# Optimization experiments

Measured on AMD Instinct MI355X. Metric: run time of the kernel, lower is better.

Reference implementation:

```python
import jax, jax.numpy as jnp
import numpy as np

D_K = 64  # hardcoded in the original module
NEG_INF = -1.0e9


def setup_inputs() -> dict:
    key = jax.random.key(0)
    kq, kk, kv = jax.random.split(key, 3)
    B, H, S, D = 2, 16, 2048, D_K
    Q = jax.random.normal(kq, (B, H, S, D), dtype=jnp.float32)
    K = jax.random.normal(kk, (B, H, S, D), dtype=jnp.float32)
    V = jax.random.normal(kv, (B, H, S, D), dtype=jnp.float32)
    # causal mask: True means masked out (matches masked_fill_ semantics)
    causal = jnp.triu(jnp.ones((S, S), dtype=jnp.bool_), k=1)
    attn_mask = jnp.broadcast_to(causal, (B, H, S, S))
    return {"Q": Q, "K": K, "V": V, "attn_mask": attn_mask}


def reference(Q, K, V, attn_mask):
    # scores = Q @ (K^T / sqrt(d_k))
    scale = 1.0 / np.sqrt(D_K).astype(np.float32)
    scores = jnp.einsum("bhqd,bhkd->bhqk", Q, K * scale)  # [B,H,S,S]
    scores = jnp.where(attn_mask, NEG_INF, scores)
    attn_scores = jax.nn.softmax(scores, axis=-1)
    context = jnp.einsum("bhqk,bhkd->bhqd", attn_scores, V)
    return (context, attn_scores)
```

## Files before the change

kernel.cpp:

```cpp
#include <hip/hip_runtime.h>
#include <stdint.h>

typedef float  f32x4  __attribute__((ext_vector_type(4)));
typedef short  s16x4  __attribute__((ext_vector_type(4)));
typedef short  s16x8  __attribute__((ext_vector_type(8)));

#define S_LEN 2048
#define D_K   64
#define NBH   32
#define VT_STRIDE (S_LEN + 32)
#define MFMA  __builtin_amdgcn_mfma_f32_16x16x32_bf16

__device__ __forceinline__ short f2bf(float f) {
    uint32_t u = __builtin_bit_cast(uint32_t, f);
    u += 0x7fffu + ((u >> 16) & 1u);
    return (short)(u >> 16);
}
__device__ __forceinline__ float bf2f(short s) {
    uint32_t u = ((uint32_t)(uint16_t)s) << 16;
    return __builtin_bit_cast(float, u);
}
__device__ __forceinline__ s16x4 cvt4(float4 f) {
    s16x4 r; r[0] = f2bf(f.x); r[1] = f2bf(f.y); r[2] = f2bf(f.z); r[3] = f2bf(f.w);
    return r;
}
__device__ __forceinline__ s16x8 cat(s16x4 a, s16x4 b) {
    return __builtin_shufflevector(a, b, 0, 1, 2, 3, 4, 5, 6, 7);
}
__device__ __forceinline__ void nt_store4(float* p, f32x4 v) {
    __builtin_nontemporal_store(v, (f32x4*)p);
}

__global__ __launch_bounds__(256) void preconv(
    const float* __restrict__ K, const float* __restrict__ V,
    short* __restrict__ Kb, short* __restrict__ VT)
{
    const int bh  = blockIdx.x >> 6;
    const int seg = blockIdx.x & 63;
    const int tid = threadIdx.x;
    const float* Ks = K + ((size_t)bh * S_LEN + seg * 32) * D_K;
    const float* Vs = V + ((size_t)bh * S_LEN + seg * 32) * D_K;
    short* Kd  = Kb + ((size_t)bh * S_LEN + seg * 32) * D_K;
    short* VTd = VT + (size_t)bh * D_K * VT_STRIDE + seg * 32;

    for (int i = tid; i < 512; i += 256) {
        const int r = i >> 4, ci = i & 15;
        float4 f = *(const float4*)(Ks + r * D_K + (ci << 2));
        const int jj = ((ci & 3) << 1) + ((ci >> 2) & 1) + ((ci >> 3) << 3);
        *(s16x4*)(Kd + r * D_K + (jj << 2)) = cvt4(f);
    }
    for (int i = tid; i < 512; i += 256) {
        const int r = i & 31, c = (i >> 5) << 2;
        float4 f = *(const float4*)(Vs + r * D_K + c);
        const int rp = (((r & 15) >> 2) << 3) + (((r >> 4) & 1) << 2) + (r & 3);
        VTd[(size_t)(c + 0) * VT_STRIDE + rp] = f2bf(f.x);
        VTd[(size_t)(c + 1) * VT_STRIDE + rp] = f2bf(f.y);
        VTd[(size_t)(c + 2) * VT_STRIDE + rp] = f2bf(f.z);
        VTd[(size_t)(c + 3) * VT_STRIDE + rp] = f2bf(f.w);
    }
}

#define SSTR 2056
__global__ __launch_bounds__(256) void attn_sp(
    const float* __restrict__ Q, const short* __restrict__ Kb,
    const short* __restrict__ VT, float* __restrict__ outC,
    float* __restrict__ outS)
{
    __shared__ __align__(16) char smem[32 * SSTR * 2];
    __shared__ float lbuf[4][32];

    const int tid = threadIdx.x, lane = tid & 63, wv = tid >> 6;
    const int xcd = blockIdx.x & 7;
    const int idx = blockIdx.x >> 3;
    const int bh  = (xcd << 2) + (idx >> 6);
    const int j   = 63 - (idx & 63);
    const int q0  = j << 5;
    const int l15 = lane & 15;
    const int g   = lane >> 4;
    const int d0  = g << 2;
    const int qa  = q0 + l15;

    const short* Kbh = Kb + (size_t)bh * S_LEN * D_K;
    const short* VTh = VT + (size_t)bh * D_K * VT_STRIDE;
    float* outSb = outS + (size_t)bh * S_LEN * S_LEN;
    float* outCb = outC + (size_t)bh * S_LEN * D_K;
    short* sstash = (short*)smem;

    s16x8 qf0a, qf1a, qf0b, qf1b;
    {
        const float4* qp = (const float4*)(Q + ((size_t)bh * S_LEN + qa) * D_K);
        qf0a = cat(cvt4(qp[g]),     cvt4(qp[g + 4]));
        qf1a = cat(cvt4(qp[g + 8]), cvt4(qp[g + 12]));
        const float4* qp2 = (const float4*)(Q + ((size_t)bh * S_LEN + qa + 16) * D_K);
        qf0b = cat(cvt4(qp2[g]),     cvt4(qp2[g + 4]));
        qf1b = cat(cvt4(qp2[g + 8]), cvt4(qp2[g + 12]));
    }

    const int ntiles = j + 1;
    const float scale = 0.125f;

    float la = 0.f, lb = 0.f;
    f32x4 z4 = {0.f,0.f,0.f,0.f};
    f32x4 cxa0 = z4, cxa1 = z4, cxa2 = z4, cxa3 = z4;
    f32x4 cxb0 = z4, cxb1 = z4, cxb2 = z4, cxb3 = z4;
    {
        s16x8 k0[4], v0[4], k1[4], v1[4];

        auto LDK = [&](s16x8* kk, s16x8* vv, int t) {
            const short* kp = Kbh + (((size_t)t << 5) + l15) * D_K + (g << 3);
            kk[0] = *(const s16x8*)(kp);
            kk[1] = *(const s16x8*)(kp + 32);
            kk[2] = *(const s16x8*)(kp + 16 * D_K);
            kk[3] = *(const s16x8*)(kp + 16 * D_K + 32);
            const short* vp = VTh + (size_t)l15 * VT_STRIDE + (t << 5) + (g << 3);
            vv[0] = *(const s16x8*)(vp);
            vv[1] = *(const s16x8*)(vp + 16 * VT_STRIDE);
            vv[2] = *(const s16x8*)(vp + 32 * VT_STRIDE);
            vv[3] = *(const s16x8*)(vp + 48 * VT_STRIDE);
        };
        auto CMPS = [&](const s16x8* kk, const s16x8* vv, int T) {
            f32x4 sa0 = z4, sa1 = z4, sb0 = z4, sb1 = z4;
            sa0 = MFMA(kk[0], qf0a, sa0, 0,0,0);
            sa0 = MFMA(kk[1], qf1a, sa0, 0,0,0);
            sa1 = MFMA(kk[2], qf0a, sa1, 0,0,0);
            sa1 = MFMA(kk[3], qf1a, sa1, 0,0,0);
            sb0 = MFMA(kk[0], qf0b, sb0, 0,0,0);
            sb0 = MFMA(kk[1], qf1b, sb0, 0,0,0);
            sb1 = MFMA(kk[2], qf0b, sb1, 0,0,0);
            sb1 = MFMA(kk[3], qf1b, sb1, 0,0,0);
            s16x8 pfa, pfb;
            if (T < j) {
                #pragma unroll
                for (int r = 0; r < 4; ++r) {
                    float e;
                    e = __expf(sa0[r] * scale); la += e; pfa[r]   = f2bf(e);
                    e = __expf(sa1[r] * scale); la += e; pfa[4+r] = f2bf(e);
                    e = __expf(sb0[r] * scale); lb += e; pfb[r]   = f2bf(e);
                    e = __expf(sb1[r] * scale); lb += e; pfb[4+r] = f2bf(e);
                }
            } else {
                #pragma unroll
                for (int r = 0; r < 4; ++r) {
                    const bool c = (d0 + r) <= l15;
                    float e;
                    e = c ? __expf(sa0[r] * scale) : 0.f; la += e; pfa[r] = f2bf(e);
                    pfa[4+r] = 0;
                    e = __expf(sb0[r] * scale);           lb += e; pfb[r] = f2bf(e);
                    e = c ? __expf(sb1[r] * scale) : 0.f; lb += e; pfb[4+r] = f2bf(e);
                }
            }
            const int cbase = (T << 5) + d0;
            short* sA = &sstash[l15 * SSTR + cbase];
            *(s16x4*)(sA)      = __builtin_shufflevector(pfa, pfa, 0, 1, 2, 3);
            *(s16x4*)(sA + 16) = __builtin_shufflevector(pfa, pfa, 4, 5, 6, 7);
            short* sB = &sstash[(16 + l15) * SSTR + cbase];
            *(s16x4*)(sB)      = __builtin_shufflevector(pfb, pfb, 0, 1, 2, 3);
            *(s16x4*)(sB + 16) = __builtin_shufflevector(pfb, pfb, 4, 5, 6, 7);
            cxa0 = MFMA(pfa, vv[0], cxa0, 0,0,0);
            cxa1 = MFMA(pfa, vv[1], cxa1, 0,0,0);
            cxa2 = MFMA(pfa, vv[2], cxa2, 0,0,0);
            cxa3 = MFMA(pfa, vv[3], cxa3, 0,0,0);
            cxb0 = MFMA(pfb, vv[0], cxb0, 0,0,0);
            cxb1 = MFMA(pfb, vv[1], cxb1, 0,0,0);
            cxb2 = MFMA(pfb, vv[2], cxb2, 0,0,0);
            cxb3 = MFMA(pfb, vv[3], cxb3, 0,0,0);
        };

        int t = wv;
        if (t < ntiles) {
            LDK(k0, v0, t);
            while (t + 4 < ntiles) {
                LDK(k1, v1, t + 4);
                CMPS(k0, v0, t);
                t += 4;
                if (t + 4 < ntiles) {
                    LDK(k0, v0, t + 4);
                    CMPS(k1, v1, t);
                    t += 4;
                } else {
                    CMPS(k1, v1, t);
                    t += 4;
                    break;
                }
            }
            if (t < ntiles) CMPS(k0, v0, t);
        }
    }
    la += __shfl_xor(la, 16); la += __shfl_xor(la, 32);
    lb += __shfl_xor(lb, 16); lb += __shfl_xor(lb, 32);
    if (lane < 16) { lbuf[wv][l15] = la; lbuf[wv][16 + l15] = lb; }
    __syncthreads();
    #pragma unroll
    for (int r = 0; r < 4; ++r) {
        const float ra = 1.f / (lbuf[0][d0 + r] + lbuf[1][d0 + r]
                              + lbuf[2][d0 + r] + lbuf[3][d0 + r]);
        const float rb = 1.f / (lbuf[0][16 + d0 + r] + lbuf[1][16 + d0 + r]
                              + lbuf[2][16 + d0 + r] + lbuf[3][16 + d0 + r]);
        cxa0[r] *= ra; cxa1[r] *= ra; cxa2[r] *= ra; cxa3[r] *= ra;
        cxb0[r] *= rb; cxb1[r] *= rb; cxb2[r] *= rb; cxb3[r] *= rb;
    }

    const int kz = ntiles << 5;
    {
        #pragma unroll
        for (int rr8 = 0; rr8 < 8; ++rr8) {
            const int row = (wv << 3) + rr8;
            const float rinv_r = 1.f /
                (lbuf[0][row] + lbuf[1][row] + lbuf[2][row] + lbuf[3][row]);
            float* rowp = outSb + (size_t)(q0 + row) * S_LEN;
            const short* srow = &sstash[row * SSTR];
            for (int c = lane << 2; c < S_LEN; c += 256) {
                f32x4 v;
                if (c < kz) {
                    s16x4 sv = *(const s16x4*)(srow + c);
                    v[0] = bf2f(sv[0]) * rinv_r;
                    v[1] = bf2f(sv[1]) * rinv_r;
                    v[2] = bf2f(sv[2]) * rinv_r;
                    v[3] = bf2f(sv[3]) * rinv_r;
                } else {
                    v[0] = 0.f; v[1] = 0.f; v[2] = 0.f; v[3] = 0.f;
                }
                nt_store4(rowp + c, v);
            }
        }
    }

    __syncthreads();
    {
        float* cb2 = (float*)smem;
        const int base = wv * 2080;
        #pragma unroll
        for (int r = 0; r < 4; ++r) {
            cb2[base + (d0 + r) * 65 +  0 + l15] = cxa0[r];
            cb2[base + (d0 + r) * 65 + 16 + l15] = cxa1[r];
            cb2[base + (d0 + r) * 65 + 32 + l15] = cxa2[r];
            cb2[base + (d0 + r) * 65 + 48 + l15] = cxa3[r];
            cb2[base + (16 + d0 + r) * 65 +  0 + l15] = cxb0[r];
            cb2[base + (16 + d0 + r) * 65 + 16 + l15] = cxb1[r];
            cb2[base + (16 + d0 + r) * 65 + 32 + l15] = cxb2[r];
            cb2[base + (16 + d0 + r) * 65 + 48 + l15] = cxb3[r];
        }
        __syncthreads();
        const int dbase = (tid & 15) << 2;
        for (int rr = tid >> 4; rr < 32; rr += 16) {
            f32x4 acc = *(const f32x4*)&cb2[0 * 2080 + rr * 65 + dbase];
            #pragma unroll
            for (int w = 1; w < 4; ++w) {
                f32x4 p = *(const f32x4*)&cb2[w * 2080 + rr * 65 + dbase];
                acc[0] += p[0]; acc[1] += p[1]; acc[2] += p[2]; acc[3] += p[3];
            }
            *(f32x4*)(outCb + (size_t)(q0 + rr) * D_K + dbase) = acc;
        }
    }
}

#define KSTRIDE 68
#define VSTRIDE 36
__global__ __launch_bounds__(256) void attn_causal_fb(
    const float* __restrict__ Q, const float* __restrict__ K,
    const float* __restrict__ V, float* __restrict__ outC,
    float* __restrict__ outS)
{
    __shared__ short Klds[32 * KSTRIDE];
    __shared__ short Vlds[64 * VSTRIDE];
    const int bh = blockIdx.x >> 5, q0 = (blockIdx.x & 31) << 6;
    const int tid = threadIdx.x, lane = tid & 63, wv = tid >> 6;
    const int q0w = q0 + (wv << 4), l15 = lane & 15, d0 = (lane >> 4) << 2;
    const int qg = q0w + l15, qhi = q0w + 15;
    const float* Kb = K + (size_t)bh * S_LEN * D_K;
    const float* Vb = V + (size_t)bh * S_LEN * D_K;
    float* outSb = outS + (size_t)bh * S_LEN * S_LEN;
    float* outCb = outC + (size_t)bh * S_LEN * D_K;
    s16x8 qf0, qf1;
    {
        const float4* qp = (const float4*)(Q + ((size_t)bh * S_LEN + qg) * D_K);
        qf0 = cat(cvt4(qp[d0 >> 2]), cvt4(qp[(d0 + 16) >> 2]));
        qf1 = cat(cvt4(qp[(d0 + 32) >> 2]), cvt4(qp[(d0 + 48) >> 2]));
    }
    const int npairs = (q0 >> 5) + 2;
    const float scale = 0.125f;
    float lsum = 0.f;
    for (int p = 0; p < npairs; ++p) {
        const int k0 = p << 5;
        for (int i = tid; i < 512; i += 256) {
            const int r = i >> 4, c = (i & 15) << 2;
            float4 f = *(const float4*)(Kb + (size_t)(k0 + r) * D_K + c);
            *(s16x4*)&Klds[r * KSTRIDE + c] = cvt4(f);
        }
        __syncthreads();
        if (k0 <= qhi) {
            #pragma unroll
            for (int s = 0; s < 2; ++s) {
                const short* kp = &Klds[(16 * s + l15) * KSTRIDE + d0];
                s16x8 a0 = cat(*(const s16x4*)kp, *(const s16x4*)(kp + 16));
                s16x8 a1 = cat(*(const s16x4*)(kp + 32), *(const s16x4*)(kp + 48));
                f32x4 c1 = {0.f,0.f,0.f,0.f};
                c1 = MFMA(a0, qf0, c1, 0,0,0);
                c1 = MFMA(a1, qf1, c1, 0,0,0);
                const int kbase = k0 + 16 * s + d0;
                #pragma unroll
                for (int r = 0; r < 4; ++r)
                    if (kbase + r <= qg) lsum += __expf(c1[r] * scale);
            }
        }
        __syncthreads();
    }
    lsum += __shfl_xor(lsum, 16);
    lsum += __shfl_xor(lsum, 32);
    const float rinv = 1.f / lsum;
    f32x4 ctx[4] = {{0,0,0,0},{0,0,0,0},{0,0,0,0},{0,0,0,0}};
    for (int p = 0; p < npairs; ++p) {
        const int k0 = p << 5;
        for (int i = tid; i < 512; i += 256) {
            const int r = i >> 4, c = (i & 15) << 2;
            float4 f = *(const float4*)(Kb + (size_t)(k0 + r) * D_K + c);
            *(s16x4*)&Klds[r * KSTRIDE + c] = cvt4(f);
            float4 gg = *(const float4*)(Vb + (size_t)(k0 + r) * D_K + c);
            Vlds[(c + 0) * VSTRIDE + r] = f2bf(gg.x);
            Vlds[(c + 1) * VSTRIDE + r] = f2bf(gg.y);
            Vlds[(c + 2) * VSTRIDE + r] = f2bf(gg.z);
            Vlds[(c + 3) * VSTRIDE + r] = f2bf(gg.w);
        }
        __syncthreads();
        if (k0 <= qhi) {
            s16x8 pf;
            #pragma unroll
            for (int s = 0; s < 2; ++s) {
                const short* kp = &Klds[(16 * s + l15) * KSTRIDE + d0];
                s16x8 a0 = cat(*(const s16x4*)kp, *(const s16x4*)(kp + 16));
                s16x8 a1 = cat(*(const s16x4*)(kp + 32), *(const s16x4*)(kp + 48));
                f32x4 c1 = {0.f,0.f,0.f,0.f};
                c1 = MFMA(a0, qf0, c1, 0,0,0);
                c1 = MFMA(a1, qf1, c1, 0,0,0);
                const int kbase = k0 + 16 * s + d0;
                f32x4 pw;
                #pragma unroll
                for (int r = 0; r < 4; ++r) {
                    float pe = (kbase + r <= qg) ? __expf(c1[r] * scale) * rinv : 0.f;
                    pw[r] = pe;
                    pf[4 * s + r] = f2bf(pe);
                }
                *(f32x4*)(outSb + (size_t)qg * S_LEN + kbase) = pw;
            }
            #pragma unroll
            for (int db = 0; db < 4; ++db) {
                const short* vp = &Vlds[(db * 16 + l15) * VSTRIDE + d0];
                s16x8 b = cat(*(const s16x4*)vp, *(const s16x4*)(vp + 16));
                ctx[db] = MFMA(pf, b, ctx[db], 0,0,0);
            }
        }
        __syncthreads();
    }
    #pragma unroll
    for (int db = 0; db < 4; ++db)
        #pragma unroll
        for (int r = 0; r < 4; ++r)
            outCb[(size_t)(q0w + d0 + r) * D_K + db * 16 + l15] = ctx[db][r];
    const int kz = ((qhi >> 5) + 1) << 5;
    const f32x4 z = {0.f,0.f,0.f,0.f};
    for (int r = 0; r < 16; ++r) {
        float* rowp = outSb + (size_t)(q0w + r) * S_LEN;
        for (int k = kz + (lane << 2); k < S_LEN; k += 256)
            *(f32x4*)(rowp + k) = z;
    }
}

extern "C" void kernel_launch(void* const* d_in, const int* in_sizes, int n_in,
                              void* d_out, int out_size, void* d_ws, size_t ws_size,
                              hipStream_t stream) {
    const float* Q = (const float*)d_in[0];
    const float* K = (const float*)d_in[1];
    const float* V = (const float*)d_in[2];
    float* outC = (float*)d_out;
    float* outS = (float*)d_out + (size_t)NBH * S_LEN * D_K;

    const size_t kb_elems = (size_t)NBH * S_LEN * D_K;
    const size_t vt_elems = (size_t)NBH * D_K * VT_STRIDE;
    const size_t need = (kb_elems + vt_elems) * sizeof(short);

    if (ws_size >= need) {
        short* Kb = (short*)d_ws;
        short* VT = Kb + kb_elems;
        preconv<<<dim3(NBH * 64), dim3(256), 0, stream>>>(K, V, Kb, VT);
        attn_sp<<<dim3(2048), dim3(256), 0, stream>>>(Q, Kb, VT, outC, outS);
    } else {
        attn_causal_fb<<<dim3(1024), dim3(256), 0, stream>>>(Q, K, V, outC, outS);
    }
}
```

Measured before the change: 147.1 us.

## Use eight waves per block to split key tiles in attention kernel

Doubles the attention block from 4 to 8 wavefronts, so each block of 32 query rows splits the key tiles across 8 waves instead of 4. The row-sum reduction, score write-out (4 rows per wave), and context reduction are rewritten for 8 partial accumulators. The context reduction runs in two phases through the shared buffer. The aim is more latency hiding and more parallelism per block on the causal workload. The cost is extra reduction and sync overhead, and possibly lower occupancy given the large shared-memory stash.

Measured after the change: 148.1 us. No clear change (+0.7%).

```diff
diff --git a/kernel.cpp b/kernel.cpp
--- a/kernel.cpp
+++ b/kernel.cpp
@@ -61,13 +61,13 @@
 }
 
 #define SSTR 2056
-__global__ __launch_bounds__(256) void attn_sp(
+__global__ __launch_bounds__(512) void attn_sp8(
     const float* __restrict__ Q, const short* __restrict__ Kb,
     const short* __restrict__ VT, float* __restrict__ outC,
     float* __restrict__ outS)
 {
     __shared__ __align__(16) char smem[32 * SSTR * 2];
-    __shared__ float lbuf[4][32];
+    __shared__ float lbuf[8][32];
 
     const int tid = threadIdx.x, lane = tid & 63, wv = tid >> 6;
     const int xcd = blockIdx.x & 7;
@@ -169,17 +169,17 @@
         int t = wv;
         if (t < ntiles) {
             LDK(k0, v0, t);
-            while (t + 4 < ntiles) {
-                LDK(k1, v1, t + 4);
+            while (t + 8 < ntiles) {
+                LDK(k1, v1, t + 8);
                 CMPS(k0, v0, t);
-                t += 4;
-                if (t + 4 < ntiles) {
-                    LDK(k0, v0, t + 4);
+                t += 8;
+                if (t + 8 < ntiles) {
+                    LDK(k0, v0, t + 8);
                     CMPS(k1, v1, t);
-                    t += 4;
+                    t += 8;
                 } else {
                     CMPS(k1, v1, t);
-                    t += 4;
+                    t += 8;
                     break;
                 }
             }
@@ -192,10 +192,13 @@
     __syncthreads();
     #pragma unroll
     for (int r = 0; r < 4; ++r) {
-        const float ra = 1.f / (lbuf[0][d0 + r] + lbuf[1][d0 + r]
-                              + lbuf[2][d0 + r] + lbuf[3][d0 + r]);
-        const float rb = 1.f / (lbuf[0][16 + d0 + r] + lbuf[1][16 + d0 + r]
-                              + lbuf[2][16 + d0 + r] + lbuf[3][16 + d0 + r]);
+        float sa = 0.f, sb = 0.f;
+        #pragma unroll
+        for (int w = 0; w < 8; ++w) {
+            sa += lbuf[w][d0 + r];
+            sb += lbuf[w][16 + d0 + r];
+        }
+        const float ra = 1.f / sa, rb = 1.f / sb;
         cxa0[r] *= ra; cxa1[r] *= ra; cxa2[r] *= ra; cxa3[r] *= ra;
         cxb0[r] *= rb; cxb1[r] *= rb; cxb2[r] *= rb; cxb3[r] *= rb;
     }
@@ -203,10 +206,12 @@
     const int kz = ntiles << 5;
     {
         #pragma unroll
-        for (int rr8 = 0; rr8 < 8; ++rr8) {
-            const int row = (wv << 3) + rr8;
-            const float rinv_r = 1.f /
-                (lbuf[0][row] + lbuf[1][row] + lbuf[2][row] + lbuf[3][row]);
+        for (int rr4 = 0; rr4 < 4; ++rr4) {
+            const int row = (wv << 2) + rr4;
+            float s = 0.f;
+            #pragma unroll
+            for (int w = 0; w < 8; ++w) s += lbuf[w][row];
+            const float rinv_r = 1.f / s;
             float* rowp = outSb + (size_t)(q0 + row) * S_LEN;
             const short* srow = &sstash[row * SSTR];
             for (int c = lane << 2; c < S_LEN; c += 256) {
@@ -228,28 +233,45 @@
     __syncthreads();
     {
         float* cb2 = (float*)smem;
-        const int base = wv * 2080;
-        #pragma unroll
-        for (int r = 0; r < 4; ++r) {
-            cb2[base + (d0 + r) * 65 +  0 + l15] = cxa0[r];
-            cb2[base + (d0 + r) * 65 + 16 + l15] = cxa1[r];
-            cb2[base + (d0 + r) * 65 + 32 + l15] = cxa2[r];
-            cb2[base + (d0 + r) * 65 + 48 + l15] = cxa3[r];
-            cb2[base + (16 + d0 + r) * 65 +  0 + l15] = cxb0[r];
-            cb2[base + (16 + d0 + r) * 65 + 16 + l15] = cxb1[r];
-            cb2[base + (16 + d0 + r) * 65 + 32 + l15] = cxb2[r];
-            cb2[base + (16 + d0 + r) * 65 + 48 + l15] = cxb3[r];
-        }
-        __syncthreads();
-        const int dbase = (tid & 15) << 2;
-        for (int rr = tid >> 4; rr < 32; rr += 16) {
-            f32x4 acc = *(const f32x4*)&cb2[0 * 2080 + rr * 65 + dbase];
+        if (wv < 4) {
+            const int base = wv * 2080;
+            #pragma unroll
+            for (int r = 0; r < 4; ++r) {
+                cb2[base + (d0 + r) * 65 +  0 + l15] = cxa0[r];
+                cb2[base + (d0 + r) * 65 + 16 + l15] = cxa1[r];
+                cb2[base + (d0 + r) * 65 + 32 + l15] = cxa2[r];
+                cb2[base + (d0 + r) * 65 + 48 + l15] = cxa3[r];
+                cb2[base + (16 + d0 + r) * 65 +  0 + l15] = cxb0[r];
+                cb2[base + (16 + d0 + r) * 65 + 16 + l15] = cxb1[r];
+                cb2[base + (16 + d0 + r) * 65 + 32 + l15] = cxb2[r];
+                cb2[base + (16 + d0 + r) * 65 + 48 + l15] = cxb3[r];
+            }
+        }
+        __syncthreads();
+        if (wv >= 4) {
+            const int base = (wv - 4) * 2080;
+            #pragma unroll
+            for (int r = 0; r < 4; ++r) {
+                cb2[base + (d0 + r) * 65 +  0 + l15] += cxa0[r];
+                cb2[base + (d0 + r) * 65 + 16 + l15] += cxa1[r];
+                cb2[base + (d0 + r) * 65 + 32 + l15] += cxa2[r];
+                cb2[base + (d0 + r) * 65 + 48 + l15] += cxa3[r];
+                cb2[base + (16 + d0 + r) * 65 +  0 + l15] += cxb0[r];
+                cb2[base + (16 + d0 + r) * 65 + 16 + l15] += cxb1[r];
+                cb2[base + (16 + d0 + r) * 65 + 32 + l15] += cxb2[r];
+                cb2[base + (16 + d0 + r) * 65 + 48 + l15] += cxb3[r];
+            }
+        }
+        __syncthreads();
+        const int row = tid >> 4, dbase = (tid & 15) << 2;
+        if (tid < 512) {
+            f32x4 acc = *(const f32x4*)&cb2[0 * 2080 + row * 65 + dbase];
             #pragma unroll
             for (int w = 1; w < 4; ++w) {
-                f32x4 p = *(const f32x4*)&cb2[w * 2080 + rr * 65 + dbase];
+                f32x4 p = *(const f32x4*)&cb2[w * 2080 + row * 65 + dbase];
                 acc[0] += p[0]; acc[1] += p[1]; acc[2] += p[2]; acc[3] += p[3];
             }
-            *(f32x4*)(outCb + (size_t)(q0 + rr) * D_K + dbase) = acc;
+            *(f32x4*)(outCb + (size_t)(q0 + row) * D_K + dbase) = acc;
         }
     }
 }
@@ -382,7 +404,7 @@
         short* Kb = (short*)d_ws;
         short* VT = Kb + kb_elems;
         preconv<<<dim3(NBH * 64), dim3(256), 0, stream>>>(K, V, Kb, VT);
-        attn_sp<<<dim3(2048), dim3(256), 0, stream>>>(Q, Kb, VT, outC, outS);
+        attn_sp8<<<dim3(2048), dim3(512), 0, stream>>>(Q, Kb, VT, outC, outS);
     } else {
         attn_causal_fb<<<dim3(1024), dim3(256), 0, stream>>>(Q, K, V, outC, outS);
     }
```

## Split attention blocks into 16-row query strips with twice as many blocks

Applied to the files above, without the earlier changes.

Each block now handles 16 query rows instead of 32, doubling the grid to 4096 blocks. The score stash shrinks to half the LDS (about 66 KB instead of 132 KB), so more blocks can be resident per CU, and work across the causal triangle is spread at a finer grain. In exchange, each K/V tile is loaded and read twice as often relative to the MFMA work it feeds, and the causal mask on the diagonal tile becomes a per-element compare.

Measured after the change: 156.2 us. 1.06x slower.

```diff
diff --git a/kernel.cpp b/kernel.cpp
--- a/kernel.cpp
+++ b/kernel.cpp
@@ -61,24 +61,24 @@
 }
 
 #define SSTR 2056
-__global__ __launch_bounds__(256) void attn_sp(
+__global__ __launch_bounds__(256) void attn_ss(
     const float* __restrict__ Q, const short* __restrict__ Kb,
     const short* __restrict__ VT, float* __restrict__ outC,
     float* __restrict__ outS)
 {
-    __shared__ __align__(16) char smem[32 * SSTR * 2];
-    __shared__ float lbuf[4][32];
+    __shared__ __align__(16) char smem[16 * SSTR * 2];
+    __shared__ float lbuf[4][16];
 
     const int tid = threadIdx.x, lane = tid & 63, wv = tid >> 6;
     const int xcd = blockIdx.x & 7;
     const int idx = blockIdx.x >> 3;
-    const int bh  = (xcd << 2) + (idx >> 6);
-    const int j   = 63 - (idx & 63);
-    const int q0  = j << 5;
+    const int bh  = (xcd << 2) + (idx >> 7);
+    const int strip = 127 - (idx & 127);
+    const int q0  = strip << 4;
     const int l15 = lane & 15;
     const int g   = lane >> 4;
     const int d0  = g << 2;
-    const int qa  = q0 + l15;
+    const int qg  = q0 + l15;
 
     const short* Kbh = Kb + (size_t)bh * S_LEN * D_K;
     const short* VTh = VT + (size_t)bh * D_K * VT_STRIDE;
@@ -86,23 +86,20 @@
     float* outCb = outC + (size_t)bh * S_LEN * D_K;
     short* sstash = (short*)smem;
 
-    s16x8 qf0a, qf1a, qf0b, qf1b;
-    {
-        const float4* qp = (const float4*)(Q + ((size_t)bh * S_LEN + qa) * D_K);
-        qf0a = cat(cvt4(qp[g]),     cvt4(qp[g + 4]));
-        qf1a = cat(cvt4(qp[g + 8]), cvt4(qp[g + 12]));
-        const float4* qp2 = (const float4*)(Q + ((size_t)bh * S_LEN + qa + 16) * D_K);
-        qf0b = cat(cvt4(qp2[g]),     cvt4(qp2[g + 4]));
-        qf1b = cat(cvt4(qp2[g + 8]), cvt4(qp2[g + 12]));
-    }
-
-    const int ntiles = j + 1;
+    s16x8 qf0, qf1;
+    {
+        const float4* qp = (const float4*)(Q + ((size_t)bh * S_LEN + qg) * D_K);
+        qf0 = cat(cvt4(qp[g]),     cvt4(qp[g + 4]));
+        qf1 = cat(cvt4(qp[g + 8]), cvt4(qp[g + 12]));
+    }
+
+    const int ntiles = (strip >> 1) + 1;
+    const int nfull  = strip >> 1;
     const float scale = 0.125f;
 
-    float la = 0.f, lb = 0.f;
+    float lsum = 0.f;
     f32x4 z4 = {0.f,0.f,0.f,0.f};
-    f32x4 cxa0 = z4, cxa1 = z4, cxa2 = z4, cxa3 = z4;
-    f32x4 cxb0 = z4, cxb1 = z4, cxb2 = z4, cxb3 = z4;
+    f32x4 cx0 = z4, cx1 = z4, cx2 = z4, cx3 = z4;
     {
         s16x8 k0[4], v0[4], k1[4], v1[4];
 
@@ -119,51 +116,38 @@
             vv[3] = *(const s16x8*)(vp + 48 * VT_STRIDE);
         };
         auto CMPS = [&](const s16x8* kk, const s16x8* vv, int T) {
-            f32x4 sa0 = z4, sa1 = z4, sb0 = z4, sb1 = z4;
-            sa0 = MFMA(kk[0], qf0a, sa0, 0,0,0);
-            sa0 = MFMA(kk[1], qf1a, sa0, 0,0,0);
-            sa1 = MFMA(kk[2], qf0a, sa1, 0,0,0);
-            sa1 = MFMA(kk[3], qf1a, sa1, 0,0,0);
-            sb0 = MFMA(kk[0], qf0b, sb0, 0,0,0);
-            sb0 = MFMA(kk[1], qf1b, sb0, 0,0,0);
-            sb1 = MFMA(kk[2], qf0b, sb1, 0,0,0);
-            sb1 = MFMA(kk[3], qf1b, sb1, 0,0,0);
-            s16x8 pfa, pfb;
-            if (T < j) {
+            f32x4 s0 = z4, s1 = z4;
+            s0 = MFMA(kk[0], qf0, s0, 0,0,0);
+            s0 = MFMA(kk[1], qf1, s0, 0,0,0);
+            s1 = MFMA(kk[2], qf0, s1, 0,0,0);
+            s1 = MFMA(kk[3], qf1, s1, 0,0,0);
+            s16x8 pf;
+            if (T < nfull) {
                 #pragma unroll
                 for (int r = 0; r < 4; ++r) {
                     float e;
-                    e = __expf(sa0[r] * scale); la += e; pfa[r]   = f2bf(e);
-                    e = __expf(sa1[r] * scale); la += e; pfa[4+r] = f2bf(e);
-                    e = __expf(sb0[r] * scale); lb += e; pfb[r]   = f2bf(e);
-                    e = __expf(sb1[r] * scale); lb += e; pfb[4+r] = f2bf(e);
+                    e = __expf(s0[r] * scale); lsum += e; pf[r]   = f2bf(e);
+                    e = __expf(s1[r] * scale); lsum += e; pf[4+r] = f2bf(e);
                 }
             } else {
+                const int kb0 = (T << 5) + d0;
                 #pragma unroll
                 for (int r = 0; r < 4; ++r) {
-                    const bool c = (d0 + r) <= l15;
                     float e;
-                    e = c ? __expf(sa0[r] * scale) : 0.f; la += e; pfa[r] = f2bf(e);
-                    pfa[4+r] = 0;
-                    e = __expf(sb0[r] * scale);           lb += e; pfb[r] = f2bf(e);
-                    e = c ? __expf(sb1[r] * scale) : 0.f; lb += e; pfb[4+r] = f2bf(e);
+                    e = (kb0 + r <= qg)      ? __expf(s0[r] * scale) : 0.f;
+                    lsum += e; pf[r] = f2bf(e);
+                    e = (kb0 + 16 + r <= qg) ? __expf(s1[r] * scale) : 0.f;
+                    lsum += e; pf[4+r] = f2bf(e);
                 }
             }
             const int cbase = (T << 5) + d0;
             short* sA = &sstash[l15 * SSTR + cbase];
-            *(s16x4*)(sA)      = __builtin_shufflevector(pfa, pfa, 0, 1, 2, 3);
-            *(s16x4*)(sA + 16) = __builtin_shufflevector(pfa, pfa, 4, 5, 6, 7);
-            short* sB = &sstash[(16 + l15) * SSTR + cbase];
-            *(s16x4*)(sB)      = __builtin_shufflevector(pfb, pfb, 0, 1, 2, 3);
-            *(s16x4*)(sB + 16) = __builtin_shufflevector(pfb, pfb, 4, 5, 6, 7);
-            cxa0 = MFMA(pfa, vv[0], cxa0, 0,0,0);
-            cxa1 = MFMA(pfa, vv[1], cxa1, 0,0,0);
-            cxa2 = MFMA(pfa, vv[2], cxa2, 0,0,0);
-            cxa3 = MFMA(pfa, vv[3], cxa3, 0,0,0);
-            cxb0 = MFMA(pfb, vv[0], cxb0, 0,0,0);
-            cxb1 = MFMA(pfb, vv[1], cxb1, 0,0,0);
-            cxb2 = MFMA(pfb, vv[2], cxb2, 0,0,0);
-            cxb3 = MFMA(pfb, vv[3], cxb3, 0,0,0);
+            *(s16x4*)(sA)      = __builtin_shufflevector(pf, pf, 0, 1, 2, 3);
+            *(s16x4*)(sA + 16) = __builtin_shufflevector(pf, pf, 4, 5, 6, 7);
+            cx0 = MFMA(pf, vv[0], cx0, 0,0,0);
+            cx1 = MFMA(pf, vv[1], cx1, 0,0,0);
+            cx2 = MFMA(pf, vv[2], cx2, 0,0,0);
+            cx3 = MFMA(pf, vv[3], cx3, 0,0,0);
         };
 
         int t = wv;
@@ -186,25 +170,22 @@
             if (t < ntiles) CMPS(k0, v0, t);
         }
     }
-    la += __shfl_xor(la, 16); la += __shfl_xor(la, 32);
-    lb += __shfl_xor(lb, 16); lb += __shfl_xor(lb, 32);
-    if (lane < 16) { lbuf[wv][l15] = la; lbuf[wv][16 + l15] = lb; }
+    lsum += __shfl_xor(lsum, 16);
+    lsum += __shfl_xor(lsum, 32);
+    if (lane < 16) lbuf[wv][l15] = lsum;
     __syncthreads();
     #pragma unroll
     for (int r = 0; r < 4; ++r) {
         const float ra = 1.f / (lbuf[0][d0 + r] + lbuf[1][d0 + r]
                               + lbuf[2][d0 + r] + lbuf[3][d0 + r]);
-        const float rb = 1.f / (lbuf[0][16 + d0 + r] + lbuf[1][16 + d0 + r]
-                              + lbuf[2][16 + d0 + r] + lbuf[3][16 + d0 + r]);
-        cxa0[r] *= ra; cxa1[r] *= ra; cxa2[r] *= ra; cxa3[r] *= ra;
-        cxb0[r] *= rb; cxb1[r] *= rb; cxb2[r] *= rb; cxb3[r] *= rb;
+        cx0[r] *= ra; cx1[r] *= ra; cx2[r] *= ra; cx3[r] *= ra;
     }
 
     const int kz = ntiles << 5;
     {
         #pragma unroll
-        for (int rr8 = 0; rr8 < 8; ++rr8) {
-            const int row = (wv << 3) + rr8;
+        for (int rr4 = 0; rr4 < 4; ++rr4) {
+            const int row = (wv << 2) + rr4;
             const float rinv_r = 1.f /
                 (lbuf[0][row] + lbuf[1][row] + lbuf[2][row] + lbuf[3][row]);
             float* rowp = outSb + (size_t)(q0 + row) * S_LEN;
@@ -228,29 +209,23 @@
     __syncthreads();
     {
         float* cb2 = (float*)smem;
-        const int base = wv * 2080;
+        const int base = wv * 1040;
         #pragma unroll
         for (int r = 0; r < 4; ++r) {
-            cb2[base + (d0 + r) * 65 +  0 + l15] = cxa0[r];
-            cb2[base + (d0 + r) * 65 + 16 + l15] = cxa1[r];
-            cb2[base + (d0 + r) * 65 + 32 + l15] = cxa2[r];
-            cb2[base + (d0 + r) * 65 + 48 + l15] = cxa3[r];
-            cb2[base + (16 + d0 + r) * 65 +  0 + l15] = cxb0[r];
-            cb2[base + (16 + d0 + r) * 65 + 16 + l15] = cxb1[r];
-            cb2[base + (16 + d0 + r) * 65 + 32 + l15] = cxb2[r];
-            cb2[base + (16 + d0 + r) * 65 + 48 + l15] = cxb3[r];
-        }
-        __syncthreads();
-        const int dbase = (tid & 15) << 2;
-        for (int rr = tid >> 4; rr < 32; rr += 16) {
-            f32x4 acc = *(const f32x4*)&cb2[0 * 2080 + rr * 65 + dbase];
-            #pragma unroll
-            for (int w = 1; w < 4; ++w) {
-                f32x4 p = *(const f32x4*)&cb2[w * 2080 + rr * 65 + dbase];
-                acc[0] += p[0]; acc[1] += p[1]; acc[2] += p[2]; acc[3] += p[3];
-            }
-            *(f32x4*)(outCb + (size_t)(q0 + rr) * D_K + dbase) = acc;
-        }
+            cb2[base + (d0 + r) * 65 +  0 + l15] = cx0[r];
+            cb2[base + (d0 + r) * 65 + 16 + l15] = cx1[r];
+            cb2[base + (d0 + r) * 65 + 32 + l15] = cx2[r];
+            cb2[base + (d0 + r) * 65 + 48 + l15] = cx3[r];
+        }
+        __syncthreads();
+        const int row = tid >> 4, dbase = (tid & 15) << 2;
+        f32x4 acc = *(const f32x4*)&cb2[0 * 1040 + row * 65 + dbase];
+        #pragma unroll
+        for (int w = 1; w < 4; ++w) {
+            f32x4 p = *(const f32x4*)&cb2[w * 1040 + row * 65 + dbase];
+            acc[0] += p[0]; acc[1] += p[1]; acc[2] += p[2]; acc[3] += p[3];
+        }
+        *(f32x4*)(outCb + (size_t)(q0 + row) * D_K + dbase) = acc;
     }
 }
 
@@ -382,7 +357,7 @@
         short* Kb = (short*)d_ws;
         short* VT = Kb + kb_elems;
         preconv<<<dim3(NBH * 64), dim3(256), 0, stream>>>(K, V, Kb, VT);
-        attn_sp<<<dim3(2048), dim3(256), 0, stream>>>(Q, Kb, VT, outC, outS);
+        attn_ss<<<dim3(4096), dim3(256), 0, stream>>>(Q, Kb, VT, outC, outS);
     } else {
         attn_causal_fb<<<dim3(1024), dim3(256), 0, stream>>>(Q, K, V, outC, outS);
     }
```
